# Kernel tuning notes

Measured on AMD Instinct MI355X. Metric: run time of the kernel, lower is better.

The kernel has to match this reference:

```python
import jax, jax.numpy as jnp
import numpy as np

T, N, E, IN_DIM, H = 20, 50000, 800000, 16, 128
NPF = 7  # num_physical_features
EPS = 1e-5


def setup_inputs() -> dict:
    key = jax.random.key(0)
    ks = jax.random.split(key, 24)
    s = 0.05
    inp = {
        'x': jax.random.normal(ks[0], (T, N, IN_DIM), jnp.float32),
        'edge_index': jax.random.randint(ks[1], (2, E), 0, N, jnp.int64),
        # SAGEConv layer 1 (PyG: lin_l on aggregated neighbors w/ bias, lin_r on root no bias)
        'sage1_wl': jax.random.normal(ks[2], (IN_DIM, H), jnp.float32) * s,
        'sage1_bl': jnp.zeros((H,), jnp.float32),
        'sage1_wr': jax.random.normal(ks[3], (IN_DIM, H), jnp.float32) * s,
        # SAGEConv layer 2
        'sage2_wl': jax.random.normal(ks[4], (H, H), jnp.float32) * s,
        'sage2_bl': jnp.zeros((H,), jnp.float32),
        'sage2_wr': jax.random.normal(ks[5], (H, H), jnp.float32) * s,
        # LayerNorm
        'ln_g': jnp.ones((H,), jnp.float32),
        'ln_b': jnp.zeros((H,), jnp.float32),
        # GRU (torch layout: [3H, H], gate order r,z,n)
        'gru_wih': jax.random.normal(ks[6], (3 * H, H), jnp.float32) * s,
        'gru_whh': jax.random.normal(ks[7], (3 * H, H), jnp.float32) * s,
        'gru_bih': jnp.zeros((3 * H,), jnp.float32),
        'gru_bhh': jnp.zeros((3 * H,), jnp.float32),
        # Thickness decoder
        'th_w1': jax.random.normal(ks[8], (H, H), jnp.float32) * s,
        'th_b1': jnp.zeros((H,), jnp.float32),
        'th_w2': jax.random.normal(ks[9], (H, 1), jnp.float32) * s,
        'th_b2': jnp.zeros((1,), jnp.float32),
        # Physical feature decoder
        'ph_w1': jax.random.normal(ks[10], (H, H), jnp.float32) * s,
        'ph_b1': jnp.zeros((H,), jnp.float32),
        'ph_w2': jax.random.normal(ks[11], (H, NPF), jnp.float32) * s,
        'ph_b2': jnp.zeros((NPF,), jnp.float32),
    }
    return inp


def _sage(h, src, dst, deg_inv, wl, bl, wr):
    # mean-aggregate neighbor features over incoming edges, then two linears
    agg = jax.ops.segment_sum(h[src], dst, num_segments=N) * deg_inv[:, None]
    return agg @ wl + bl + h @ wr


def _forward(x, edge_index,
             sage1_wl, sage1_bl, sage1_wr,
             sage2_wl, sage2_bl, sage2_wr,
             ln_g, ln_b,
             gru_wih, gru_whh, gru_bih, gru_bhh,
             th_w1, th_b1, th_w2, th_b2,
             ph_w1, ph_b1, ph_w2, ph_b2):
    src, dst = edge_index[0], edge_index[1]
    deg = jax.ops.segment_sum(jnp.ones((E,), jnp.float32), dst, num_segments=N)
    deg_inv = 1.0 / jnp.maximum(deg, 1.0)

    def encode(xt):  # [N, IN_DIM] -> [N, H]
        h = jax.nn.relu(_sage(xt, src, dst, deg_inv, sage1_wl, sage1_bl, sage1_wr))
        h = jax.nn.relu(_sage(h, src, dst, deg_inv, sage2_wl, sage2_bl, sage2_wr))
        mu = jnp.mean(h, axis=-1, keepdims=True)
        var = jnp.mean(jnp.square(h - mu), axis=-1, keepdims=True)
        return (h - mu) * jax.lax.rsqrt(var + EPS) * ln_g + ln_b

    encoded = jax.lax.map(encode, x)  # [T, N, H]

    # GRU over time, batch = nodes
    def gru_step(h, x_t):
        gi = x_t @ gru_wih.T + gru_bih  # [N, 3H]
        gh = h @ gru_whh.T + gru_bhh
        i_r, i_z, i_n = jnp.split(gi, 3, axis=-1)
        h_r, h_z, h_n = jnp.split(gh, 3, axis=-1)
        r = jax.nn.sigmoid(i_r + h_r)
        z = jax.nn.sigmoid(i_z + h_z)
        n = jnp.tanh(i_n + r * h_n)
        h_new = (1.0 - z) * n + z * h
        return h_new, h_new

    h0 = jnp.zeros((N, H), jnp.float32)
    _, h_temporal = jax.lax.scan(gru_step, h0, encoded)  # [T, N, H]

    th = jax.nn.relu(h_temporal @ th_w1 + th_b1) @ th_w2 + th_b2   # [T, N, 1]
    ph = jax.nn.relu(h_temporal @ ph_w1 + ph_b1) @ ph_w2 + ph_b2   # [T, N, NPF]
    return th, ph


def reference(x, edge_index,
              sage1_wl, sage1_bl, sage1_wr,
              sage2_wl, sage2_bl, sage2_wr,
              ln_g, ln_b,
              gru_wih, gru_whh, gru_bih, gru_bhh,
              th_w1, th_b1, th_w2, th_b2,
              ph_w1, ph_b1, ph_w2, ph_b2):
    return _forward(x, edge_index,
                    sage1_wl, sage1_bl, sage1_wr,
                    sage2_wl, sage2_bl, sage2_wr,
                    ln_g, ln_b,
                    gru_wih, gru_whh, gru_bih, gru_bhh,
                    th_w1, th_b1, th_w2, th_b2,
                    ph_w1, ph_b1, ph_w2, ph_b2)
```

## Files before the change

kernel.cpp:

```cpp
#include <hip/hip_runtime.h>
#include <hip/hip_bf16.h>

#define TT 20
#define NN 50000
#define EE 800000
#define IND 16
#define HH 128
#define NPF 7
#define CC 4
#define NB ((NN + 255) / 256)

typedef __attribute__((ext_vector_type(8))) short bf16x8;
typedef __attribute__((ext_vector_type(4))) float f32x4;
#define MFMA(a, b, c) __builtin_amdgcn_mfma_f32_16x16x32_bf16(a, b, c, 0, 0, 0)

__device__ __forceinline__ unsigned short f2bf(float f) {
    union { float f; unsigned u; } v; v.f = f;
    unsigned r = v.u + 0x7fffu + ((v.u >> 16) & 1u);
    return (unsigned short)(r >> 16);
}
__device__ __forceinline__ float bf2f(unsigned short u) {
    union { unsigned u; float f; } v; v.u = ((unsigned)u) << 16;
    return v.f;
}

__global__ void detect_kernel(const int* ei, int* flag, int E) {
    __shared__ int nz;
    if (threadIdx.x == 0) nz = 0;
    __syncthreads();
    for (int i = threadIdx.x; i < 1024 && i < E; i += blockDim.x)
        if (ei[2 * i + 1] != 0) atomicOr(&nz, 1);
    __syncthreads();
    if (threadIdx.x == 0) *flag = (nz == 0) ? 1 : 0;
}
__device__ __forceinline__ int edge_src(const int* ei, int e, int E, int f) {
    return f ? ei[2 * e] : ei[e];
}
__device__ __forceinline__ int edge_dst(const int* ei, int e, int E, int f) {
    return f ? ei[2 * (E + e)] : ei[E + e];
}
__global__ void count_deg_kernel(const int* ei, const int* flag, int* deg, int E) {
    int e = blockIdx.x * blockDim.x + threadIdx.x;
    if (e >= E) return;
    int f = *flag;
    atomicAdd(&deg[edge_dst(ei, e, E, f)], 1);
}

__global__ __launch_bounds__(256) void sum_blocks_kernel(const int* deg, int* bsum) {
    int i = blockIdx.x * 256 + threadIdx.x;
    int v = (i < NN) ? deg[i] : 0;
#pragma unroll
    for (int o = 1; o <= 32; o <<= 1) v += __shfl_xor(v, o);
    __shared__ int ws[4];
    if ((threadIdx.x & 63) == 0) ws[threadIdx.x >> 6] = v;
    __syncthreads();
    if (threadIdx.x == 0) bsum[blockIdx.x] = ws[0] + ws[1] + ws[2] + ws[3];
}
__global__ __launch_bounds__(256) void scan_blocks_kernel(const int* bsum, int* bbase) {
    __shared__ int arr[256];
    int t = threadIdx.x;
    int v = (t < NB) ? bsum[t] : 0;
    arr[t] = v;
    __syncthreads();
    for (int off = 1; off < 256; off <<= 1) {
        int u = (t >= off) ? arr[t - off] : 0;
        __syncthreads();
        arr[t] += u;
        __syncthreads();
    }
    if (t < NB) bbase[t] = arr[t] - v;
}
__global__ __launch_bounds__(256) void offs_kernel(const int* deg, const int* bbase,
                                                   int* offs, int* cursor,
                                                   float* dinv, int E) {
    __shared__ int arr[256];
    int t = threadIdx.x;
    int i = blockIdx.x * 256 + t;
    int d = (i < NN) ? deg[i] : 0;
    arr[t] = d;
    __syncthreads();
    for (int off = 1; off < 256; off <<= 1) {
        int u = (t >= off) ? arr[t - off] : 0;
        __syncthreads();
        arr[t] += u;
        __syncthreads();
    }
    if (i < NN) {
        int o = bbase[blockIdx.x] + arr[t] - d;
        offs[i] = o;
        cursor[i] = o;
        dinv[i] = 1.0f / (float)(d > 1 ? d : 1);
        if (i == NN - 1) offs[NN] = E;
    }
}
__global__ void fill_csr_kernel(const int* ei, const int* flag, int* cursor,
                                int* csr, int E) {
    int e = blockIdx.x * blockDim.x + threadIdx.x;
    if (e >= E) return;
    int f = *flag;
    int s = edge_src(ei, e, E, f);
    int d = edge_dst(ei, e, E, f);
    int p = atomicAdd(&cursor[d], 1);
    csr[p] = s;
}

__global__ void pack_all_kernel(
    const float* s2wl, const float* s2wr, const float* tw1, const float* pw1,
    const float* wih, const float* whh,
    unsigned short* pS2L, unsigned short* pS2R, unsigned short* pT1,
    unsigned short* pP1, unsigned short* pGI, unsigned short* pGH) {
    int id = blockIdx.x * blockDim.x + threadIdx.x;
    if (id >= 80 * 256) return;
    int gt = id >> 8;
    int lane = id & 63, kk = (id >> 6) & 3;
    const float* src; unsigned short* dst; int tile, mode, ncols;
    if (gt < 8)       { src = s2wl; dst = pS2L; tile = gt;      mode = 0; ncols = 128; }
    else if (gt < 16) { src = s2wr; dst = pS2R; tile = gt - 8;  mode = 0; ncols = 128; }
    else if (gt < 24) { src = tw1;  dst = pT1;  tile = gt - 16; mode = 0; ncols = 128; }
    else if (gt < 32) { src = pw1;  dst = pP1;  tile = gt - 24; mode = 0; ncols = 128; }
    else if (gt < 56) { src = wih;  dst = pGI;  tile = gt - 32; mode = 1; ncols = 384; }
    else              { src = whh;  dst = pGH;  tile = gt - 56; mode = 1; ncols = 384; }
    int n = tile * 16 + (lane & 15);
    int kbase = kk * 32 + (lane >> 4) * 8;
    unsigned short out[8];
#pragma unroll
    for (int i = 0; i < 8; ++i) {
        int k = kbase + i;
        float v = mode ? src[n * HH + k] : src[k * ncols + n];
        out[i] = f2bf(v);
    }
    *(uint4*)(dst + ((size_t)tile * 256 + kk * 64 + lane) * 8) = *(uint4*)out;
}

__global__ __launch_bounds__(128) void sage1_kernel(
    const float* __restrict__ x, const int* __restrict__ offs,
    const int* __restrict__ csr, const float* __restrict__ dinv,
    const float* __restrict__ wl, const float* __restrict__ bl,
    const float* __restrict__ wr, unsigned short* __restrict__ h1c, int t0) {
    const int tid = threadIdx.x;
    const int ci = blockIdx.y;
    const float* xt = x + (size_t)(t0 + ci) * NN * IND;
    const int m0 = blockIdx.x * 8;
    __shared__ __align__(16) float sAgg[8][IND];
    __shared__ float sX[8][IND];
    {
        int r = tid >> 4, node = m0 + r;
        int l16 = tid & 15, sub = l16 >> 2, q = l16 & 3;
        int e1 = offs[node + 1];
        float4 a0 = make_float4(0.f, 0.f, 0.f, 0.f);
        float4 a1 = make_float4(0.f, 0.f, 0.f, 0.f);
        float4 a2 = make_float4(0.f, 0.f, 0.f, 0.f);
        float4 a3 = make_float4(0.f, 0.f, 0.f, 0.f);
        int e = offs[node] + sub;
        for (; e + 12 < e1; e += 16) {
            int s0 = __builtin_nontemporal_load(&csr[e]);
            int s1 = __builtin_nontemporal_load(&csr[e + 4]);
            int s2 = __builtin_nontemporal_load(&csr[e + 8]);
            int s3 = __builtin_nontemporal_load(&csr[e + 12]);
            float4 v0 = *(const float4*)(xt + (size_t)s0 * IND + q * 4);
            float4 v1 = *(const float4*)(xt + (size_t)s1 * IND + q * 4);
            float4 v2 = *(const float4*)(xt + (size_t)s2 * IND + q * 4);
            float4 v3 = *(const float4*)(xt + (size_t)s3 * IND + q * 4);
            a0.x += v0.x; a0.y += v0.y; a0.z += v0.z; a0.w += v0.w;
            a1.x += v1.x; a1.y += v1.y; a1.z += v1.z; a1.w += v1.w;
            a2.x += v2.x; a2.y += v2.y; a2.z += v2.z; a2.w += v2.w;
            a3.x += v3.x; a3.y += v3.y; a3.z += v3.z; a3.w += v3.w;
        }
        for (; e < e1; e += 4) {
            int s0 = __builtin_nontemporal_load(&csr[e]);
            float4 v0 = *(const float4*)(xt + (size_t)s0 * IND + q * 4);
            a0.x += v0.x; a0.y += v0.y; a0.z += v0.z; a0.w += v0.w;
        }
        float4 acc;
        acc.x = a0.x + a1.x + a2.x + a3.x;
        acc.y = a0.y + a1.y + a2.y + a3.y;
        acc.z = a0.z + a1.z + a2.z + a3.z;
        acc.w = a0.w + a1.w + a2.w + a3.w;
#pragma unroll
        for (int o = 4; o <= 8; o <<= 1) {
            acc.x += __shfl_xor(acc.x, o);
            acc.y += __shfl_xor(acc.y, o);
            acc.z += __shfl_xor(acc.z, o);
            acc.w += __shfl_xor(acc.w, o);
        }
        if (sub == 0) {
            float di = dinv[node];
            acc.x *= di; acc.y *= di; acc.z *= di; acc.w *= di;
            *(float4*)&sAgg[r][q * 4] = acc;
        }
        sX[r][l16] = xt[(size_t)node * IND + l16];
    }
    __syncthreads();
    const int col = tid;
    float acc[8];
    float b = bl[col];
#pragma unroll
    for (int m = 0; m < 8; ++m) acc[m] = b;
#pragma unroll
    for (int k = 0; k < IND; ++k) {
        float wlv = wl[k * HH + col];
        float wrv = wr[k * HH + col];
#pragma unroll
        for (int m = 0; m < 8; ++m) acc[m] += sAgg[m][k] * wlv + sX[m][k] * wrv;
    }
#pragma unroll
    for (int m = 0; m < 8; ++m)
        h1c[((size_t)(m0 + m) * CC + ci) * HH + col] = f2bf(fmaxf(acc[m], 0.f));
}

#define ADD8(acc, v) do {                                     \
    union { unsigned u; float f; } t_;                        \
    t_.u = (v).x << 16;         acc[0] += t_.f;               \
    t_.u = (v).x & 0xffff0000u; acc[1] += t_.f;               \
    t_.u = (v).y << 16;         acc[2] += t_.f;               \
    t_.u = (v).y & 0xffff0000u; acc[3] += t_.f;               \
    t_.u = (v).z << 16;         acc[4] += t_.f;               \
    t_.u = (v).z & 0xffff0000u; acc[5] += t_.f;               \
    t_.u = (v).w << 16;         acc[6] += t_.f;               \
    t_.u = (v).w & 0xffff0000u; acc[7] += t_.f;               \
} while (0)

__global__ __launch_bounds__(256) void sage2_agg_kernel(
    const unsigned short* __restrict__ h1c, const int* __restrict__ offs,
    const int* __restrict__ csr, const float* __restrict__ dinv,
    unsigned short* __restrict__ agg2c) {
    const int wid = threadIdx.x >> 6, lane = threadIdx.x & 63;
    const int n = blockIdx.x * 4 + wid;
    const char* __restrict__ tb = (const char*)h1c;
    const int lb = lane * 16;
    const int e0 = offs[n], e1 = offs[n + 1];
    float a[8] = {0,0,0,0,0,0,0,0}, b[8] = {0,0,0,0,0,0,0,0};
    float c_[8] = {0,0,0,0,0,0,0,0}, d[8] = {0,0,0,0,0,0,0,0};
    int e = e0;
    for (; e + 3 < e1; e += 4) {
        int s0 = csr[e], s1 = csr[e + 1], s2 = csr[e + 2], s3 = csr[e + 3];
        uint4 v0 = *(const uint4*)(tb + (size_t)s0 * 1024 + lb);
        uint4 v1 = *(const uint4*)(tb + (size_t)s1 * 1024 + lb);
        uint4 v2 = *(const uint4*)(tb + (size_t)s2 * 1024 + lb);
        uint4 v3 = *(const uint4*)(tb + (size_t)s3 * 1024 + lb);
        ADD8(a, v0); ADD8(b, v1); ADD8(c_, v2); ADD8(d, v3);
    }
    for (; e < e1; ++e) {
        int s0 = csr[e];
        uint4 v0 = *(const uint4*)(tb + (size_t)s0 * 1024 + lb);
        ADD8(a, v0);
    }
    float di = dinv[n];
    unsigned short o[8];
#pragma unroll
    for (int j = 0; j < 8; ++j) o[j] = f2bf((a[j] + b[j] + c_[j] + d[j]) * di);
    *(uint4*)((char*)agg2c + (size_t)n * 1024 + lb) = *(uint4*)o;
}

#define LDA(buf, kk)                                                          \
    (*(const bf16x8*)((const char*)(buf) +                                    \
        (((lane & 15) * 256 + (kk) * 64 + (lane >> 4) * 16) ^                 \
         (((lane & 15) & 7) << 4))))

__global__ __launch_bounds__(64, 4) void gru_fused_kernel(
    const unsigned short* __restrict__ agg2c, const unsigned short* __restrict__ h1c,
    const unsigned short* __restrict__ pS2L, const unsigned short* __restrict__ pS2R,
    const float* __restrict__ s2bl, const float* __restrict__ lng,
    const float* __restrict__ lnb,
    const unsigned short* __restrict__ pGI, const unsigned short* __restrict__ pGH,
    const float* __restrict__ bih, const float* __restrict__ bhh,
    float* __restrict__ h, unsigned short* __restrict__ hallc, int ci) {
    const int lane = threadIdx.x;
    const int r0 = blockIdx.x * 16;
    __shared__ unsigned short bufA[16 * 128];
    __shared__ unsigned short bufB[16 * 128];

#pragma unroll
    for (int j = 0; j < 4; ++j) {
        int off = (lane + 64 * j) * 16;
        int row = off >> 8, colb = off & 255;
        int swz = off ^ ((row & 7) << 4);
        size_t src = (size_t)(r0 + row) * 1024 + (size_t)ci * 256 + colb;
        *(uint4*)((char*)bufA + swz) = *(const uint4*)((const char*)agg2c + src);
        *(uint4*)((char*)bufB + swz) = *(const uint4*)((const char*)h1c + src);
    }
    __syncthreads();

    bf16x8 ae[4], ah[4];
#pragma unroll
    for (int kk = 0; kk < 4; ++kk) { ae[kk] = LDA(bufA, kk); ah[kk] = LDA(bufB, kk); }
    __syncthreads();

#pragma unroll
    for (int j = 0; j < 4; ++j) {
        int off = (lane + 64 * j) * 16;
        int row = off >> 8;
        int swz = off ^ ((row & 7) << 4);
        const float* hs = h + (size_t)r0 * HH + (size_t)(off / 2);
        unsigned short tmp[8];
#pragma unroll
        for (int i = 0; i < 8; ++i) tmp[i] = f2bf(hs[i]);
        *(uint4*)((char*)bufB + swz) = *(uint4*)tmp;
    }

    float vE[8][4];
    float sS[4] = {0, 0, 0, 0}, sQ[4] = {0, 0, 0, 0};
#pragma unroll
    for (int c = 0; c < 8; ++c) {
        f32x4 al = {0, 0, 0, 0}, ar = {0, 0, 0, 0};
#pragma unroll
        for (int kk = 0; kk < 4; ++kk) {
            bf16x8 bl = *(const bf16x8*)(pS2L + ((size_t)(c * 4 + kk) * 64 + lane) * 8);
            bf16x8 br = *(const bf16x8*)(pS2R + ((size_t)(c * 4 + kk) * 64 + lane) * 8);
            al = MFMA(ae[kk], bl, al);
            ar = MFMA(ah[kk], br, ar);
        }
        int col = c * 16 + (lane & 15);
        float bb = s2bl[col];
#pragma unroll
        for (int j = 0; j < 4; ++j) {
            float v = fmaxf(al[j] + ar[j] + bb, 0.f);
            vE[c][j] = v; sS[j] += v; sQ[j] += v * v;
        }
    }
#pragma unroll
    for (int o = 1; o <= 8; o <<= 1) {
#pragma unroll
        for (int j = 0; j < 4; ++j) {
            sS[j] += __shfl_xor(sS[j], o);
            sQ[j] += __shfl_xor(sQ[j], o);
        }
    }
    __syncthreads();
#pragma unroll
    for (int c = 0; c < 8; ++c) {
        int col = c * 16 + (lane & 15);
        float g = lng[col], b = lnb[col];
#pragma unroll
        for (int j = 0; j < 4; ++j) {
            float mu = sS[j] * (1.f / 128.f);
            float var = sQ[j] * (1.f / 128.f) - mu * mu;
            float ve = (vE[c][j] - mu) * rsqrtf(var + 1e-5f) * g + b;
            int row = (lane >> 4) * 4 + j;
            int off = ((row * 128 + col) * 2) ^ ((row & 7) << 4);
            *(unsigned short*)((char*)bufA + off) = f2bf(ve);
        }
    }
    __syncthreads();

    bf16x8 xe[4], xh[4];
#pragma unroll
    for (int kk = 0; kk < 4; ++kk) { xe[kk] = LDA(bufA, kk); xh[kk] = LDA(bufB, kk); }
#pragma unroll
    for (int c = 0; c < 8; ++c) {
        f32x4 air = {0,0,0,0}, aiz = {0,0,0,0}, ain = {0,0,0,0};
        f32x4 ahr = {0,0,0,0}, ahz = {0,0,0,0}, ahn = {0,0,0,0};
#pragma unroll
        for (int kk = 0; kk < 4; ++kk) {
            bf16x8 bir = *(const bf16x8*)(pGI + ((size_t)((c     ) * 4 + kk) * 64 + lane) * 8);
            bf16x8 biz = *(const bf16x8*)(pGI + ((size_t)((c +  8) * 4 + kk) * 64 + lane) * 8);
            bf16x8 bin = *(const bf16x8*)(pGI + ((size_t)((c + 16) * 4 + kk) * 64 + lane) * 8);
            bf16x8 bhr = *(const bf16x8*)(pGH + ((size_t)((c     ) * 4 + kk) * 64 + lane) * 8);
            bf16x8 bhz = *(const bf16x8*)(pGH + ((size_t)((c +  8) * 4 + kk) * 64 + lane) * 8);
            bf16x8 bhn = *(const bf16x8*)(pGH + ((size_t)((c + 16) * 4 + kk) * 64 + lane) * 8);
            air = MFMA(xe[kk], bir, air); aiz = MFMA(xe[kk], biz, aiz);
            ain = MFMA(xe[kk], bin, ain);
            ahr = MFMA(xh[kk], bhr, ahr); ahz = MFMA(xh[kk], bhz, ahz);
            ahn = MFMA(xh[kk], bhn, ahn);
        }
        int col = c * 16 + (lane & 15);
        float bir_ = bih[col], biz_ = bih[HH + col], bin_ = bih[2 * HH + col];
        float bhr_ = bhh[col], bhz_ = bhh[HH + col], bhn_ = bhh[2 * HH + col];
#pragma unroll
        for (int j = 0; j < 4; ++j) {
            int row = (lane >> 4) * 4 + j;
            size_t gidx = (size_t)(r0 + row) * HH + col;
            float rr = 1.f / (1.f + expf(-(air[j] + bir_ + ahr[j] + bhr_)));
            float zz = 1.f / (1.f + expf(-(aiz[j] + biz_ + ahz[j] + bhz_)));
            float nn2 = tanhf(ain[j] + bin_ + rr * (ahn[j] + bhn_));
            float hold = h[gidx];
            float hnew = (1.f - zz) * nn2 + zz * hold;
            h[gidx] = hnew;
            hallc[((size_t)(r0 + row) * CC + ci) * HH + col] = f2bf(hnew);
        }
    }
}

__global__ __launch_bounds__(64) void dec_kernel(
    const unsigned short* __restrict__ hall,
    const unsigned short* __restrict__ pT1, const unsigned short* __restrict__ pP1,
    const float* __restrict__ tb1, const float* __restrict__ tw2,
    const float* __restrict__ tb2, const float* __restrict__ pb1,
    const float* __restrict__ pw2, const float* __restrict__ pb2,
    float* __restrict__ out_th, float* __restrict__ out_ph, int t0) {
    const int lane = threadIdx.x;
    const int rc = blockIdx.x * 16;
    const int ci = rc / NN;
    const int n0 = rc - ci * NN;
    const int tg = t0 + ci;
    __shared__ unsigned short bufB[16 * 128];
#pragma unroll
    for (int j = 0; j < 4; ++j) {
        int off = (lane + 64 * j) * 16;
        int row = off >> 8, colb = off & 255;
        int swz = off ^ ((row & 7) << 4);
        *(uint4*)((char*)bufB + swz) =
            *(const uint4*)((const char*)hall +
                            (size_t)(n0 + row) * 1024 + (size_t)ci * 256 + colb);
    }
    __syncthreads();
    bf16x8 xd[4];
#pragma unroll
    for (int kk = 0; kk < 4; ++kk) xd[kk] = LDA(bufB, kk);
    float pt[4] = {0, 0, 0, 0};
    float pf[NPF][4];
#pragma unroll
    for (int f = 0; f < NPF; ++f)
#pragma unroll
        for (int j = 0; j < 4; ++j) pf[f][j] = 0.f;
#pragma unroll
    for (int c = 0; c < 8; ++c) {
        f32x4 at = {0, 0, 0, 0}, ap = {0, 0, 0, 0};
#pragma unroll
        for (int kk = 0; kk < 4; ++kk) {
            bf16x8 bt = *(const bf16x8*)(pT1 + ((size_t)(c * 4 + kk) * 64 + lane) * 8);
            bf16x8 bp = *(const bf16x8*)(pP1 + ((size_t)(c * 4 + kk) * 64 + lane) * 8);
            at = MFMA(xd[kk], bt, at);
            ap = MFMA(xd[kk], bp, ap);
        }
        int col = c * 16 + (lane & 15);
        float b1 = tb1[col], b2 = pb1[col], w2 = tw2[col];
        float wp[NPF];
#pragma unroll
        for (int f = 0; f < NPF; ++f) wp[f] = pw2[col * NPF + f];
#pragma unroll
        for (int j = 0; j < 4; ++j) {
            float a = fmaxf(at[j] + b1, 0.f);
            pt[j] += a * w2;
            float p = fmaxf(ap[j] + b2, 0.f);
#pragma unroll
            for (int f = 0; f < NPF; ++f) pf[f][j] += p * wp[f];
        }
    }
#pragma unroll
    for (int o = 1; o <= 8; o <<= 1) {
#pragma unroll
        for (int j = 0; j < 4; ++j) {
            pt[j] += __shfl_xor(pt[j], o);
#pragma unroll
            for (int f = 0; f < NPF; ++f) pf[f][j] += __shfl_xor(pf[f][j], o);
        }
    }
    if ((lane & 15) == 0) {
        int g = lane >> 4;
#pragma unroll
        for (int j = 0; j < 4; ++j) {
            int gr = n0 + g * 4 + j;
            out_th[(size_t)tg * NN + gr] = pt[j] + tb2[0];
#pragma unroll
            for (int f = 0; f < NPF; ++f)
                out_ph[((size_t)tg * NN + gr) * NPF + f] = pf[f][j] + pb2[f];
        }
    }
}
#undef LDA

extern "C" void kernel_launch(void* const* d_in, const int* in_sizes, int n_in,
                              void* d_out, int out_size, void* d_ws, size_t ws_size,
                              hipStream_t stream) {
    const float* x     = (const float*)d_in[0];
    const int*   ei    = (const int*)d_in[1];
    const float* s1wl  = (const float*)d_in[2];
    const float* s1bl  = (const float*)d_in[3];
    const float* s1wr  = (const float*)d_in[4];
    const float* s2wl  = (const float*)d_in[5];
    const float* s2bl  = (const float*)d_in[6];
    const float* s2wr  = (const float*)d_in[7];
    const float* lng   = (const float*)d_in[8];
    const float* lnb   = (const float*)d_in[9];
    const float* g_wih = (const float*)d_in[10];
    const float* g_whh = (const float*)d_in[11];
    const float* g_bih = (const float*)d_in[12];
    const float* g_bhh = (const float*)d_in[13];
    const float* tw1   = (const float*)d_in[14];
    const float* tb1   = (const float*)d_in[15];
    const float* tw2   = (const float*)d_in[16];
    const float* tb2   = (const float*)d_in[17];
    const float* pw1   = (const float*)d_in[18];
    const float* pb1   = (const float*)d_in[19];
    const float* pw2   = (const float*)d_in[20];
    const float* pb2   = (const float*)d_in[21];

    char* ws = (char*)d_ws;
    size_t o = 0;
    auto alloc = [&](size_t bytes) {
        size_t r = o;
        o += (bytes + 255) & ~(size_t)255;
        return r;
    };
    int*            flag  = (int*)(ws + alloc(4));
    int*            deg   = (int*)(ws + alloc((size_t)NN * 4));
    int*            offs  = (int*)(ws + alloc((size_t)(NN + 1) * 4));
    int*            curs  = (int*)(ws + alloc((size_t)NN * 4));
    int*            csr   = (int*)(ws + alloc((size_t)EE * 4));
    float*          dinv  = (float*)(ws + alloc((size_t)NN * 4));
    int*            bsum  = (int*)(ws + alloc((size_t)NB * 4));
    int*            bbase = (int*)(ws + alloc((size_t)NB * 4));
    unsigned short* pS2L  = (unsigned short*)(ws + alloc(8 * 4 * 64 * 8 * 2));
    unsigned short* pS2R  = (unsigned short*)(ws + alloc(8 * 4 * 64 * 8 * 2));
    unsigned short* pT1   = (unsigned short*)(ws + alloc(8 * 4 * 64 * 8 * 2));
    unsigned short* pP1   = (unsigned short*)(ws + alloc(8 * 4 * 64 * 8 * 2));
    unsigned short* pGI   = (unsigned short*)(ws + alloc(24 * 4 * 64 * 8 * 2));
    unsigned short* pGH   = (unsigned short*)(ws + alloc(24 * 4 * 64 * 8 * 2));
    float*          hbuf  = (float*)(ws + alloc((size_t)NN * HH * 4));
    unsigned short* h1c   = (unsigned short*)(ws + alloc((size_t)NN * CC * HH * 2));
    unsigned short* agg2c = (unsigned short*)(ws + alloc((size_t)NN * CC * HH * 2));
    unsigned short* hallc = agg2c;

    detect_kernel<<<1, 256, 0, stream>>>(ei, flag, EE);
    hipMemsetAsync(deg, 0, (size_t)NN * 4, stream);
    count_deg_kernel<<<(EE + 255) / 256, 256, 0, stream>>>(ei, flag, deg, EE);
    sum_blocks_kernel<<<NB, 256, 0, stream>>>(deg, bsum);
    scan_blocks_kernel<<<1, 256, 0, stream>>>(bsum, bbase);
    offs_kernel<<<NB, 256, 0, stream>>>(deg, bbase, offs, curs, dinv, EE);
    fill_csr_kernel<<<(EE + 255) / 256, 256, 0, stream>>>(ei, flag, curs, csr, EE);
    pack_all_kernel<<<(80 * 256 + 255) / 256, 256, 0, stream>>>(
        s2wl, s2wr, tw1, pw1, g_wih, g_whh, pS2L, pS2R, pT1, pP1, pGI, pGH);
    hipMemsetAsync(hbuf, 0, (size_t)NN * HH * 4, stream);

    float* out = (float*)d_out;
    for (int t0 = 0; t0 < TT; t0 += CC) {
        dim3 g1(NN / 8, CC);
        sage1_kernel<<<g1, 128, 0, stream>>>(x, offs, csr, dinv, s1wl, s1bl,
                                             s1wr, h1c, t0);
        sage2_agg_kernel<<<NN / 4, 256, 0, stream>>>(h1c, offs, csr, dinv, agg2c);
        for (int ci = 0; ci < CC; ++ci) {
            gru_fused_kernel<<<NN / 16, 64, 0, stream>>>(
                agg2c, h1c, pS2L, pS2R, s2bl, lng, lnb, pGI, pGH,
                g_bih, g_bhh, hbuf, hallc, ci);
        }
        dec_kernel<<<CC * NN / 16, 64, 0, stream>>>(
            hallc, pT1, pP1, tb1, tw2, tb2, pb1, pw2, pb2,
            out, out + (size_t)TT * NN, t0);
    }
}
```

Before: 2.358 ms.

## Interleave timestep chunk features per node and split SAGE1 into gather and GEMM

Adds a transpose kernel that packs the four timesteps of a chunk into a node-major [N,64] buffer. A separate aggregation kernel then gathers all four timesteps per neighbour with one 256-byte row read, which amortises the CSR index reads and the random-access cost across timesteps. The small SAGE1 GEMM now reads the precomputed aggregates and features. This adds two extra launches and extra global traffic for the staging buffers, which alias the agg2c workspace.

New measurement: 2.300 ms, median of 2. 1.02x faster.

```diff
diff --git a/kernel.cpp b/kernel.cpp
--- a/kernel.cpp
+++ b/kernel.cpp
@@ -132,63 +132,49 @@
     *(uint4*)(dst + ((size_t)tile * 256 + kk * 64 + lane) * 8) = *(uint4*)out;
 }
 
-__global__ __launch_bounds__(128) void sage1_kernel(
-    const float* __restrict__ x, const int* __restrict__ offs,
+__global__ __launch_bounds__(256) void xi_kernel(
+    const float* __restrict__ x, float* __restrict__ xi, int t0) {
+    int id = blockIdx.x * 256 + threadIdx.x;
+    if (id >= NN * 16) return;
+    int n = id >> 4, r4 = id & 15;
+    int ci = r4 >> 2, f4 = (r4 & 3) * 4;
+    float4 v = *(const float4*)(x + ((size_t)(t0 + ci) * NN + n) * IND + f4);
+    *(float4*)(xi + (size_t)n * 64 + ci * 16 + f4) = v;
+}
+
+__global__ __launch_bounds__(256) void sage1_agg_kernel(
+    const float* __restrict__ xi, const int* __restrict__ offs,
     const int* __restrict__ csr, const float* __restrict__ dinv,
+    float* __restrict__ agg1) {
+    const int wid = threadIdx.x >> 6, lane = threadIdx.x & 63;
+    const int n = blockIdx.x * 4 + wid;
+    const int e0 = offs[n], e1 = offs[n + 1];
+    float a0 = 0.f, a1 = 0.f, a2 = 0.f, a3 = 0.f;
+    int e = e0;
+    for (; e + 3 < e1; e += 4) {
+        int s0 = csr[e], s1 = csr[e + 1], s2 = csr[e + 2], s3 = csr[e + 3];
+        a0 += xi[(size_t)s0 * 64 + lane];
+        a1 += xi[(size_t)s1 * 64 + lane];
+        a2 += xi[(size_t)s2 * 64 + lane];
+        a3 += xi[(size_t)s3 * 64 + lane];
+    }
+    for (; e < e1; ++e) a0 += xi[(size_t)csr[e] * 64 + lane];
+    agg1[(size_t)n * 64 + lane] = (a0 + a1 + a2 + a3) * dinv[n];
+}
+
+__global__ __launch_bounds__(128) void sage1_gemm_kernel(
+    const float* __restrict__ agg1, const float* __restrict__ xi,
     const float* __restrict__ wl, const float* __restrict__ bl,
-    const float* __restrict__ wr, unsigned short* __restrict__ h1c, int t0) {
+    const float* __restrict__ wr, unsigned short* __restrict__ h1c) {
     const int tid = threadIdx.x;
     const int ci = blockIdx.y;
-    const float* xt = x + (size_t)(t0 + ci) * NN * IND;
     const int m0 = blockIdx.x * 8;
     __shared__ __align__(16) float sAgg[8][IND];
-    __shared__ float sX[8][IND];
+    __shared__ __align__(16) float sX[8][IND];
     {
-        int r = tid >> 4, node = m0 + r;
-        int l16 = tid & 15, sub = l16 >> 2, q = l16 & 3;
-        int e1 = offs[node + 1];
-        float4 a0 = make_float4(0.f, 0.f, 0.f, 0.f);
-        float4 a1 = make_float4(0.f, 0.f, 0.f, 0.f);
-        float4 a2 = make_float4(0.f, 0.f, 0.f, 0.f);
-        float4 a3 = make_float4(0.f, 0.f, 0.f, 0.f);
-        int e = offs[node] + sub;
-        for (; e + 12 < e1; e += 16) {
-            int s0 = __builtin_nontemporal_load(&csr[e]);
-            int s1 = __builtin_nontemporal_load(&csr[e + 4]);
-            int s2 = __builtin_nontemporal_load(&csr[e + 8]);
-            int s3 = __builtin_nontemporal_load(&csr[e + 12]);
-            float4 v0 = *(const float4*)(xt + (size_t)s0 * IND + q * 4);
-            float4 v1 = *(const float4*)(xt + (size_t)s1 * IND + q * 4);
-            float4 v2 = *(const float4*)(xt + (size_t)s2 * IND + q * 4);
-            float4 v3 = *(const float4*)(xt + (size_t)s3 * IND + q * 4);
-            a0.x += v0.x; a0.y += v0.y; a0.z += v0.z; a0.w += v0.w;
-            a1.x += v1.x; a1.y += v1.y; a1.z += v1.z; a1.w += v1.w;
-            a2.x += v2.x; a2.y += v2.y; a2.z += v2.z; a2.w += v2.w;
-            a3.x += v3.x; a3.y += v3.y; a3.z += v3.z; a3.w += v3.w;
-        }
-        for (; e < e1; e += 4) {
-            int s0 = __builtin_nontemporal_load(&csr[e]);
-            float4 v0 = *(const float4*)(xt + (size_t)s0 * IND + q * 4);
-            a0.x += v0.x; a0.y += v0.y; a0.z += v0.z; a0.w += v0.w;
-        }
-        float4 acc;
-        acc.x = a0.x + a1.x + a2.x + a3.x;
-        acc.y = a0.y + a1.y + a2.y + a3.y;
-        acc.z = a0.z + a1.z + a2.z + a3.z;
-        acc.w = a0.w + a1.w + a2.w + a3.w;
-#pragma unroll
-        for (int o = 4; o <= 8; o <<= 1) {
-            acc.x += __shfl_xor(acc.x, o);
-            acc.y += __shfl_xor(acc.y, o);
-            acc.z += __shfl_xor(acc.z, o);
-            acc.w += __shfl_xor(acc.w, o);
-        }
-        if (sub == 0) {
-            float di = dinv[node];
-            acc.x *= di; acc.y *= di; acc.z *= di; acc.w *= di;
-            *(float4*)&sAgg[r][q * 4] = acc;
-        }
-        sX[r][l16] = xt[(size_t)node * IND + l16];
+        int r = tid >> 4, f = tid & 15;
+        sAgg[r][f] = agg1[(size_t)(m0 + r) * 64 + ci * 16 + f];
+        sX[r][f]   = xi[(size_t)(m0 + r) * 64 + ci * 16 + f];
     }
     __syncthreads();
     const int col = tid;
@@ -511,6 +497,8 @@
     unsigned short* h1c   = (unsigned short*)(ws + alloc((size_t)NN * CC * HH * 2));
     unsigned short* agg2c = (unsigned short*)(ws + alloc((size_t)NN * CC * HH * 2));
     unsigned short* hallc = agg2c;
+    float*          xi    = (float*)agg2c;
+    float*          agg1  = (float*)((char*)agg2c + (size_t)NN * 64 * 4);
 
     detect_kernel<<<1, 256, 0, stream>>>(ei, flag, EE);
     hipMemsetAsync(deg, 0, (size_t)NN * 4, stream);
@@ -525,9 +513,10 @@
 
     float* out = (float*)d_out;
     for (int t0 = 0; t0 < TT; t0 += CC) {
-        dim3 g1(NN / 8, CC);
-        sage1_kernel<<<g1, 128, 0, stream>>>(x, offs, csr, dinv, s1wl, s1bl,
-                                             s1wr, h1c, t0);
+        dim3 gg(NN / 8, CC);
+        xi_kernel<<<(NN * 16 + 255) / 256, 256, 0, stream>>>(x, xi, t0);
+        sage1_agg_kernel<<<NN / 4, 256, 0, stream>>>(xi, offs, csr, dinv, agg1);
+        sage1_gemm_kernel<<<gg, 128, 0, stream>>>(agg1, xi, s1wl, s1bl, s1wr, h1c);
         sage2_agg_kernel<<<NN / 4, 256, 0, stream>>>(h1c, offs, csr, dinv, agg2c);
         for (int ci = 0; ci < CC; ++ci) {
             gru_fused_kernel<<<NN / 16, 64, 0, stream>>>(
```
